# Optimization experiments

Hardware: AMD Instinct MI355X
Metric: run time of the kernel (lower is better)

The kernel has to match this reference:

```python
import jax, jax.numpy as jnp
import numpy as np


def setup_inputs() -> dict:
    key = jax.random.key(0)
    k1, k2 = jax.random.split(key)
    B, C, H, W = 8, 64, 256, 256
    x = jax.random.normal(k1, (B, C, H, W), dtype=jnp.float32)
    # per-pixel, channel-shared 5x5 dynamic kernel: [25, B, 1, H, W]
    weights = jax.random.normal(k2, (25, B, 1, H, W), dtype=jnp.float32)
    return {"x": x, "weights": weights}


def reference(x, weights):
    # x: [B, C, H, W]; weights: [25, B, 1, H, W]
    B, C, H, W = x.shape
    PAD = 2  # 5x5 window -> pad 2 on each side (zeros)
    xp = jnp.pad(x, ((0, 0), (0, 0), (PAD, PAD), (PAD, PAD)))
    Z = jnp.zeros_like(x)
    k = 0
    for hh in range(5):  # fixed small structural loop (25 taps)
        for ww in range(5):
            Z = Z + xp[:, :, hh:hh + H, ww:ww + W] * weights[k]
            k += 1
    return Z
```

## Files before the change

### kernel.cpp

```cpp
#include <hip/hip_runtime.h>

#define B_ 8
#define C_ 64
#define H_ 256
#define W_ 256
#define ST 32
#define NCH 4
#define WSTR (B_ * H_ * W_)

__global__ __launch_bounds__(256) void kpn5x5_v3(const float* __restrict__ x,
                                                 const float* __restrict__ wgt,
                                                 float* __restrict__ out) {
  const int tid  = threadIdx.x;
  const int lane = tid & 63;
  const int wv   = tid >> 6;
  const int w0   = blockIdx.x * 64;
  const int h0   = blockIdx.y * ST;
  const int bz   = blockIdx.z;
  const int b    = bz & 7;
  const int c0   = (bz >> 3) * 16 + wv * NCH;

  int   voff[5];
  float msk[5];
#pragma unroll
  for (int d = 0; d < 5; ++d) {
    const int col = w0 + lane - 2 + d;
    const bool ok = (col >= 0) && (col < W_);
    voff[d] = ok ? col : 0;
    msk[d]  = ok ? 1.0f : 0.0f;
  }

  const float* xc = x + (size_t)(b * C_ + c0) * (H_ * W_);
  float win[NCH][5][5];
  float wc[25];

#pragma unroll
  for (int i = 0; i < 4; ++i) {
    const int r = h0 - 2 + i;
    if ((unsigned)r < (unsigned)H_) {
#pragma unroll
      for (int ch = 0; ch < NCH; ++ch) {
        const float* p = xc + (size_t)ch * (H_ * W_) + (size_t)r * W_;
#pragma unroll
        for (int d = 0; d < 5; ++d) win[ch][i][d] = p[voff[d]] * msk[d];
      }
    } else {
#pragma unroll
      for (int ch = 0; ch < NCH; ++ch)
#pragma unroll
        for (int d = 0; d < 5; ++d) win[ch][i][d] = 0.0f;
    }
  }

  {
    const float* wq = wgt + ((size_t)b * H_ + h0) * W_ + w0;
#pragma unroll
    for (int k = 0; k < 25; ++k) wc[k] = wq[(size_t)k * WSTR + lane];
  }

#define STEP(U) do {                                                        \
    const int h_  = hb + (U);                                               \
    const int rb_ = h_ + 2;                                                 \
    if (rb_ < H_) {                                                         \
      _Pragma("unroll")                                                     \
      for (int ch = 0; ch < NCH; ++ch) {                                    \
        const float* p_ = xc + (size_t)ch * (H_ * W_) + (size_t)rb_ * W_;   \
        _Pragma("unroll")                                                   \
        for (int d = 0; d < 5; ++d)                                         \
          win[ch][((U) + 4) % 5][d] = p_[voff[d]] * msk[d];                 \
      }                                                                     \
    } else {                                                                \
      _Pragma("unroll")                                                     \
      for (int ch = 0; ch < NCH; ++ch)                                      \
        _Pragma("unroll")                                                   \
        for (int d = 0; d < 5; ++d) win[ch][((U) + 4) % 5][d] = 0.0f;       \
    }                                                                       \
    float a_[NCH];                                                          \
    _Pragma("unroll")                                                       \
    for (int ch = 0; ch < NCH; ++ch) a_[ch] = 0.0f;                         \
    _Pragma("unroll")                                                       \
    for (int i = 0; i < 5; ++i)                                             \
      _Pragma("unroll")                                                     \
      for (int d = 0; d < 5; ++d) {                                         \
        const float wt_ = wc[i * 5 + d];                                    \
        _Pragma("unroll")                                                   \
        for (int ch = 0; ch < NCH; ++ch)                                    \
          a_[ch] += win[ch][((U) + i) % 5][d] * wt_;                        \
      }                                                                     \
    {                                                                       \
      const size_t ob_ = ((size_t)(b * C_ + c0) * H_ + (h0 + sb + (U)))     \
                           * W_ + w0 + lane;                                \
      _Pragma("unroll")                                                     \
      for (int ch = 0; ch < NCH; ++ch)                                      \
        out[ob_ + (size_t)ch * (H_ * W_)] = a_[ch];                         \
    }                                                                       \
    {                                                                       \
      int hw_ = h_ + 1; if (hw_ > H_ - 1) hw_ = H_ - 1;                     \
      const float* wq_ = wgt + ((size_t)b * H_ + hw_) * W_ + w0;            \
      _Pragma("unroll")                                                     \
      for (int k = 0; k < 25; ++k) wc[k] = wq_[(size_t)k * WSTR + lane];    \
    }                                                                       \
  } while (0)

  int hb = h0, sb = 0;
  for (int g = 0; g < 3; ++g) {
    STEP(0); STEP(1); STEP(2); STEP(3); STEP(4);
    STEP(5); STEP(6); STEP(7); STEP(8); STEP(9);
    hb += 10; sb += 10;
  }
  STEP(0); STEP(1);
#undef STEP
}

extern "C" void kernel_launch(void* const* d_in, const int* in_sizes, int n_in,
                              void* d_out, int out_size, void* d_ws, size_t ws_size,
                              hipStream_t stream) {
  const float* x   = (const float*)d_in[0];
  const float* wgt = (const float*)d_in[1];
  float* out = (float*)d_out;
  dim3 grid(W_ / 64, H_ / ST, (C_ / (NCH * 4)) * B_);
  dim3 block(256);
  kpn5x5_v3<<<grid, block, 0, stream>>>(x, wgt, out);
}
```

Measured before the change: 334.4 us.

## Restructure 5x5 KPN to scatter-style accumulation with one input row in registers

Each step now loads one new input row and scatters it into five rolling output accumulators, instead of keeping a five-row input window and gathering from it. This cuts input register storage and reorders weight loads to follow the scatter. It also adds launch bounds targeting 4 blocks per CU, forces the base pointers into scalar registers with readfirstlane, and writes the output with nontemporal stores. In exchange it keeps 20 accumulators live and makes the weight-load order more complex, which could raise latency or register pressure.

```diff
diff --git a/kernel.cpp b/kernel.cpp
--- a/kernel.cpp
+++ b/kernel.cpp
@@ -6,11 +6,12 @@
 #define W_ 256
 #define ST 32
 #define NCH 4
+#define HW (H_ * W_)
 #define WSTR (B_ * H_ * W_)
 
-__global__ __launch_bounds__(256) void kpn5x5_v3(const float* __restrict__ x,
-                                                 const float* __restrict__ wgt,
-                                                 float* __restrict__ out) {
+__global__ __launch_bounds__(256, 4) void kpn5x5_v5(const float* __restrict__ x,
+                                                    const float* __restrict__ wgt,
+                                                    float* __restrict__ out) {
   const int tid  = threadIdx.x;
   const int lane = tid & 63;
   const int wv   = tid >> 6;
@@ -30,85 +31,122 @@
     msk[d]  = ok ? 1.0f : 0.0f;
   }
 
-  const float* xc = x + (size_t)(b * C_ + c0) * (H_ * W_);
-  float win[NCH][5][5];
-  float wc[25];
+  const float* xc;
+  float* oc;
+  {
+    uint64_t px = (uint64_t)(x + (size_t)(b * C_ + c0) * HW);
+    px = ((uint64_t)(uint32_t)__builtin_amdgcn_readfirstlane((int)(px >> 32)) << 32) |
+         (uint64_t)(uint32_t)__builtin_amdgcn_readfirstlane((int)px);
+    xc = (const float*)px;
+    uint64_t po = (uint64_t)(out + (size_t)(b * C_ + c0) * HW);
+    po = ((uint64_t)(uint32_t)__builtin_amdgcn_readfirstlane((int)(po >> 32)) << 32) |
+         (uint64_t)(uint32_t)__builtin_amdgcn_readfirstlane((int)po);
+    oc = (float*)po;
+  }
+  const float* wq = wgt + (size_t)b * HW + w0;
+
+  float cur[NCH][5];
+  float pf[NCH][5];
+  float wcs[5][5];
+  float acc[NCH][5];
 
 #pragma unroll
-  for (int i = 0; i < 4; ++i) {
-    const int r = h0 - 2 + i;
-    if ((unsigned)r < (unsigned)H_) {
+  for (int ch = 0; ch < NCH; ++ch)
+#pragma unroll
+    for (int s = 0; s < 5; ++s) acc[ch][s] = 0.0f;
+
+  {
+    const int r = h0 - 2;
+    if (r >= 0) {
 #pragma unroll
       for (int ch = 0; ch < NCH; ++ch) {
-        const float* p = xc + (size_t)ch * (H_ * W_) + (size_t)r * W_;
+        const float* p = xc + ch * HW + r * W_;
 #pragma unroll
-        for (int d = 0; d < 5; ++d) win[ch][i][d] = p[voff[d]] * msk[d];
+        for (int d = 0; d < 5; ++d) pf[ch][d] = p[voff[d]];
       }
     } else {
 #pragma unroll
       for (int ch = 0; ch < NCH; ++ch)
 #pragma unroll
-        for (int d = 0; d < 5; ++d) win[ch][i][d] = 0.0f;
+        for (int d = 0; d < 5; ++d) pf[ch][d] = 0.0f;
+    }
+#pragma unroll
+    for (int j = 0; j < 5; ++j) {
+      const int s = (4 - j) % 5;
+      int hh = h0 - j;
+      if (hh < 0) hh = 0;
+      const float* p = wq + (size_t)hh * W_;
+#pragma unroll
+      for (int d = 0; d < 5; ++d)
+        wcs[s][d] = p[(size_t)(j * 5 + d) * WSTR + lane];
     }
   }
 
-  {
-    const float* wq = wgt + ((size_t)b * H_ + h0) * W_ + w0;
-#pragma unroll
-    for (int k = 0; k < 25; ++k) wc[k] = wq[(size_t)k * WSTR + lane];
-  }
-
-#define STEP(U) do {                                                        \
-    const int h_  = hb + (U);                                               \
-    const int rb_ = h_ + 2;                                                 \
-    if (rb_ < H_) {                                                         \
-      _Pragma("unroll")                                                     \
-      for (int ch = 0; ch < NCH; ++ch) {                                    \
-        const float* p_ = xc + (size_t)ch * (H_ * W_) + (size_t)rb_ * W_;   \
-        _Pragma("unroll")                                                   \
-        for (int d = 0; d < 5; ++d)                                         \
-          win[ch][((U) + 4) % 5][d] = p_[voff[d]] * msk[d];                 \
-      }                                                                     \
-    } else {                                                                \
-      _Pragma("unroll")                                                     \
-      for (int ch = 0; ch < NCH; ++ch)                                      \
-        _Pragma("unroll")                                                   \
-        for (int d = 0; d < 5; ++d) win[ch][((U) + 4) % 5][d] = 0.0f;       \
-    }                                                                       \
-    float a_[NCH];                                                          \
-    _Pragma("unroll")                                                       \
-    for (int ch = 0; ch < NCH; ++ch) a_[ch] = 0.0f;                         \
-    _Pragma("unroll")                                                       \
-    for (int i = 0; i < 5; ++i)                                             \
-      _Pragma("unroll")                                                     \
-      for (int d = 0; d < 5; ++d) {                                         \
-        const float wt_ = wc[i * 5 + d];                                    \
-        _Pragma("unroll")                                                   \
-        for (int ch = 0; ch < NCH; ++ch)                                    \
-          a_[ch] += win[ch][((U) + i) % 5][d] * wt_;                        \
-      }                                                                     \
-    {                                                                       \
-      const size_t ob_ = ((size_t)(b * C_ + c0) * H_ + (h0 + sb + (U)))     \
-                           * W_ + w0 + lane;                                \
-      _Pragma("unroll")                                                     \
-      for (int ch = 0; ch < NCH; ++ch)                                      \
-        out[ob_ + (size_t)ch * (H_ * W_)] = a_[ch];                         \
-    }                                                                       \
-    {                                                                       \
-      int hw_ = h_ + 1; if (hw_ > H_ - 1) hw_ = H_ - 1;                     \
-      const float* wq_ = wgt + ((size_t)b * H_ + hw_) * W_ + w0;            \
-      _Pragma("unroll")                                                     \
-      for (int k = 0; k < 25; ++k) wc[k] = wq_[(size_t)k * WSTR + lane];    \
-    }                                                                       \
+#define STEP(S, UO, DOST) do {                                               \
+    const int u_ = ub + (UO);                                                \
+    _Pragma("unroll")                                                        \
+    for (int ch = 0; ch < NCH; ++ch)                                         \
+      _Pragma("unroll")                                                      \
+      for (int d = 0; d < 5; ++d) cur[ch][d] = pf[ch][d] * msk[d];           \
+    {                                                                        \
+      const int rb = h0 - 1 + u_;                                            \
+      if ((unsigned)rb < (unsigned)H_) {                                     \
+        _Pragma("unroll")                                                    \
+        for (int ch = 0; ch < NCH; ++ch) {                                   \
+          const float* p_ = xc + ch * HW + rb * W_;                          \
+          _Pragma("unroll")                                                  \
+          for (int d = 0; d < 5; ++d) pf[ch][d] = p_[voff[d]];               \
+        }                                                                    \
+      } else {                                                               \
+        _Pragma("unroll")                                                    \
+        for (int ch = 0; ch < NCH; ++ch)                                     \
+          _Pragma("unroll")                                                  \
+          for (int d = 0; d < 5; ++d) pf[ch][d] = 0.0f;                      \
+      }                                                                      \
+    }                                                                        \
+    _Pragma("unroll")                                                        \
+    for (int j = 0; j < 5; ++j) {                                            \
+      const int s_ = ((S) + 4 - j) % 5;                                      \
+      _Pragma("unroll")                                                      \
+      for (int d = 0; d < 5; ++d) {                                          \
+        const float wt_ = wcs[s_][d];                                        \
+        _Pragma("unroll")                                                    \
+        for (int ch = 0; ch < NCH; ++ch)                                     \
+          acc[ch][s_] += cur[ch][d] * wt_;                                   \
+      }                                                                      \
+      if (j == 4) {                                                          \
+        if (DOST) {                                                          \
+          const size_t ob_ = (size_t)(h0 + u_ - 4) * W_ + w0 + lane;         \
+          _Pragma("unroll")                                                  \
+          for (int ch = 0; ch < NCH; ++ch)                                   \
+            __builtin_nontemporal_store(acc[ch][(S)],                        \
+                                        &oc[ob_ + (size_t)ch * HW]);         \
+        }                                                                    \
+        _Pragma("unroll")                                                    \
+        for (int ch = 0; ch < NCH; ++ch) acc[ch][(S)] = 0.0f;                \
+      }                                                                      \
+      {                                                                      \
+        int wr_ = (j == 4) ? (h0 + u_ + 1) : (h0 + u_ - j);                  \
+        const int tb_ = (j == 4) ? 0 : (j + 1) * 5;                          \
+        if (wr_ < 0) wr_ = 0;                                                \
+        if (wr_ > H_ - 1) wr_ = H_ - 1;                                      \
+        const float* pw_ = wq + (size_t)wr_ * W_;                            \
+        _Pragma("unroll")                                                    \
+        for (int d = 0; d < 5; ++d)                                          \
+          wcs[s_][d] = pw_[(size_t)(tb_ + d) * WSTR + lane];                 \
+      }                                                                      \
+    }                                                                        \
   } while (0)
 
-  int hb = h0, sb = 0;
-  for (int g = 0; g < 3; ++g) {
-    STEP(0); STEP(1); STEP(2); STEP(3); STEP(4);
-    STEP(5); STEP(6); STEP(7); STEP(8); STEP(9);
-    hb += 10; sb += 10;
+  int ub = 0;
+  STEP(0, 0, false); STEP(1, 1, false); STEP(2, 2, false); STEP(3, 3, false);
+  ub = 4;
+  for (int g = 0; g < 6; ++g) {
+    STEP(4, 0, true); STEP(0, 1, true); STEP(1, 2, true);
+    STEP(2, 3, true); STEP(3, 4, true);
+    ub += 5;
   }
-  STEP(0); STEP(1);
+  STEP(4, 0, true); STEP(0, 1, true);
 #undef STEP
 }
 
@@ -120,5 +158,5 @@
   float* out = (float*)d_out;
   dim3 grid(W_ / 64, H_ / ST, (C_ / (NCH * 4)) * B_);
   dim3 block(256);
-  kpn5x5_v3<<<grid, block, 0, stream>>>(x, wgt, out);
+  kpn5x5_v5<<<grid, block, 0, stream>>>(x, wgt, out);
 }
```

Result: slower. 854.8 us (+155.6%).
